# Performance work log

Measured on AMD Instinct MI355X. Metric: run time of the kernel, lower is better.

The kernel has to match this reference:

```python
import jax, jax.numpy as jnp
import numpy as np

PH = PW = 16  # patch size


def setup_inputs() -> dict:
    key = jax.random.key(0)
    k1, k2, k3, k4, k5 = jax.random.split(key, 5)
    B, N, D, V = 8, 4096, 768, 10240
    x = jax.random.uniform(k1, (B, N, D), dtype=jnp.float32)          # (B, N, ph*pw*C) in [0,1)
    patch_coord = jax.random.randint(k2, (B, N, 2), 0, 64).astype(jnp.int64)  # (y, x) grid coords
    patch_valid = jax.random.randint(k3, (B, N), 0, 2).astype(bool)
    proj_w = jax.random.normal(k4, (D, D), dtype=jnp.float32) * 0.02  # Linear weight (out, in), no bias
    pos_table = jax.random.normal(k5, (2, V, D), dtype=jnp.float32) * 0.02
    return {"x": x, "patch_coord": patch_coord, "patch_valid": patch_valid,
            "proj_w": proj_w, "pos_table": pos_table}


def reference(x, patch_coord, patch_valid, proj_w, pos_table):
    B, N, PPC = x.shape
    C = PPC // (PH * PW)
    # Reorder patch pixels from (ph, pw, C) flat order to (C, ph, pw) flat order.
    x = x.reshape(B, N, PH, PW, C).transpose(0, 1, 4, 2, 3).reshape(B, N, PPC)
    x = 2.0 * (x - 0.5)
    x = jnp.einsum('bnk,dk->bnd', x, proj_w)  # Linear, bias=False
    # External (y, x) -> internal (x, y)
    position_ids = patch_coord[..., ::-1]
    clamped = jnp.maximum(position_ids, 0)
    # Equivalent to one_hot(clamped) @ table summed over the 2 coord axes.
    pos = pos_table[0][clamped[..., 0]] + pos_table[1][clamped[..., 1]]  # (B, N, D)
    padding_positions = ~patch_valid
    pos = jnp.where(padding_positions[..., None], 0.0, pos)
    return x + pos, position_ids, padding_positions
```

## Files before the change

### kernel.cpp

```cpp
#include <hip/hip_runtime.h>
#include <hip/hip_bf16.h>
#include <cstddef>

#define D_DIM 768
#define V_DIM 10240
#define ROWS  32768
#define BM    64
#define BK    32
#define KTILES (D_DIM / BK)

using bf16x8 = __attribute__((ext_vector_type(8))) __bf16;
using bf16x4 = __attribute__((ext_vector_type(4))) __bf16;
using f32x4  = __attribute__((ext_vector_type(4))) float;

__global__ void prep_w(const float* __restrict__ W, __bf16* __restrict__ Wp,
                       float* __restrict__ bias) {
    __shared__ float row[D_DIM];
    __shared__ float red[256];
    const int d = blockIdx.x;
    const int t = threadIdx.x;
    float s = 0.f;
    for (int k = t; k < D_DIM; k += 256) {
        float w = W[(size_t)d * D_DIM + k];
        row[k] = w;
        s += w;
    }
    red[t] = s;
    __syncthreads();
    for (int off = 128; off > 0; off >>= 1) {
        if (t < off) red[t] += red[t + off];
        __syncthreads();
    }
    if (t == 0) bias[d] = -red[0];
    for (int j = t; j < D_DIM; j += 256) {
        int c  = j % 3;
        int pw = (j / 3) & 15;
        int ph = j / 48;
        Wp[(size_t)d * D_DIM + j] = (__bf16)(2.0f * row[c * 256 + ph * 16 + pw]);
    }
}

__launch_bounds__(512, 2)
__global__ void gemm_fused(const float* __restrict__ X, const __bf16* __restrict__ Wp,
                           const float* __restrict__ bias, const float* __restrict__ ptab,
                           const int* __restrict__ coord, const int* __restrict__ valid,
                           float* __restrict__ out0, float* __restrict__ out1,
                           float* __restrict__ out2) {
    __shared__ __align__(16) __bf16 la[2][BM * BK];
    __shared__ __align__(16) __bf16 lb[2][D_DIM * BK];

    const int tid  = threadIdx.x;
    const int lane = tid & 63;
    const int wave = tid >> 6;
    const int wr   = (wave >> 2) * 32;
    const int wc   = (wave & 3) * 192;
    const int lr   = lane & 15;
    const int qh   = lane >> 4;

    const int m0 = blockIdx.x * BM;

    if (tid < BM) {
        int m  = m0 + tid;
        int c0 = coord[2 * m];
        int c1 = coord[2 * m + 1];
        out1[2 * m]     = (float)c1;
        out1[2 * m + 1] = (float)c0;
        out2[m] = valid[m] ? 0.0f : 1.0f;
    }

    const __bf16* bsrc[6];
    int bdst[6];
    #pragma unroll
    for (int i = 0; i < 6; ++i) {
        int q   = i * 512 + tid;
        int row = q >> 2;
        int su  = (q & 3) ^ ((row >> 1) & 3);
        bsrc[i] = Wp + (size_t)row * D_DIM + su * 8;
        bdst[i] = q * 8;
    }

    const int a_row = tid >> 3;
    const int a_u   = (tid & 7) >> 1;
    const int a_h   = tid & 1;
    const int a_off = a_row * BK + (a_u ^ ((a_row >> 1) & 3)) * 8 + a_h * 4;
    const float* aptr = X + (size_t)(m0 + a_row) * D_DIM + ((tid & 7) << 2);

    int aoff[2], boff[12];
    #pragma unroll
    for (int i = 0; i < 2; ++i) {
        int row = wr + i * 16 + lr;
        aoff[i] = row * BK + (qh ^ ((row >> 1) & 3)) * 8;
    }
    #pragma unroll
    for (int j = 0; j < 12; ++j) {
        int row = wc + j * 16 + lr;
        boff[j] = row * BK + (qh ^ ((row >> 1) & 3)) * 8;
    }

    f32x4 acc[2][12] = {};

    #pragma unroll
    for (int i = 0; i < 6; ++i)
        __builtin_amdgcn_global_load_lds(
            (const __attribute__((address_space(1))) void*)bsrc[i],
            (__attribute__((address_space(3))) void*)&lb[0][bdst[i]], 16, 0, 0);
    {
        float4 f = *(const float4*)aptr;
        bf16x4 v;
        v[0] = (__bf16)f.x; v[1] = (__bf16)f.y; v[2] = (__bf16)f.z; v[3] = (__bf16)f.w;
        *(bf16x4*)&la[0][a_off] = v;
    }
    __syncthreads();

    for (int kt = 0; kt < KTILES; ++kt) {
        const int cur = kt & 1;
        const int nxt = cur ^ 1;
        const int k1  = (kt + 1) * BK;

        float4 fA;
        if (kt + 1 < KTILES) {
            #pragma unroll
            for (int i = 0; i < 6; ++i)
                __builtin_amdgcn_global_load_lds(
                    (const __attribute__((address_space(1))) void*)(bsrc[i] + k1),
                    (__attribute__((address_space(3))) void*)&lb[nxt][bdst[i]], 16, 0, 0);
            fA = *(const float4*)(aptr + k1);
        }

        bf16x8 af0 = *(const bf16x8*)&la[cur][aoff[0]];
        bf16x8 af1 = *(const bf16x8*)&la[cur][aoff[1]];

        #pragma unroll
        for (int j = 0; j < 12; ++j) {
            bf16x8 bfv = *(const bf16x8*)&lb[cur][boff[j]];
            acc[0][j] = __builtin_amdgcn_mfma_f32_16x16x32_bf16(af0, bfv, acc[0][j], 0, 0, 0);
            acc[1][j] = __builtin_amdgcn_mfma_f32_16x16x32_bf16(af1, bfv, acc[1][j], 0, 0, 0);
        }

        if (kt + 1 < KTILES) {
            bf16x4 v;
            v[0] = (__bf16)fA.x; v[1] = (__bf16)fA.y; v[2] = (__bf16)fA.z; v[3] = (__bf16)fA.w;
            *(bf16x4*)&la[nxt][a_off] = v;
        }
        __syncthreads();
    }

    const float* pt0 = ptab;
    const float* pt1 = ptab + (size_t)V_DIM * D_DIM;

    float bv[12];
    #pragma unroll
    for (int j = 0; j < 12; ++j)
        bv[j] = bias[wc + j * 16 + lr];

    #pragma unroll
    for (int i = 0; i < 2; ++i) {
        #pragma unroll
        for (int r = 0; r < 4; ++r) {
            const int m = m0 + wr + i * 16 + qh * 4 + r;
            int c0 = coord[2 * m];
            int c1 = coord[2 * m + 1];
            if (c0 < 0) c0 = 0;
            if (c1 < 0) c1 = 0;
            const int vld = valid[m];
            const float* p0 = pt0 + (size_t)c1 * D_DIM;
            const float* p1 = pt1 + (size_t)c0 * D_DIM;
            float* orow = out0 + (size_t)m * D_DIM;
            #pragma unroll
            for (int j = 0; j < 12; ++j) {
                const int d = wc + j * 16 + lr;
                float v = acc[i][j][r] + bv[j];
                if (vld)
                    v += p0[d] + p1[d];
                orow[d] = v;
            }
        }
    }
}

extern "C" void kernel_launch(void* const* d_in, const int* in_sizes, int n_in,
                              void* d_out, int out_size, void* d_ws, size_t ws_size,
                              hipStream_t stream) {
    const float* x     = (const float*)d_in[0];
    const int*   coord = (const int*)d_in[1];
    const int*   valid = (const int*)d_in[2];
    const float* W     = (const float*)d_in[3];
    const float* ptab  = (const float*)d_in[4];

    float* out0 = (float*)d_out;
    float* out1 = out0 + (size_t)ROWS * D_DIM;
    float* out2 = out1 + (size_t)ROWS * 2;

    __bf16* Wp   = (__bf16*)d_ws;
    float*  bias = (float*)((char*)d_ws + (size_t)D_DIM * D_DIM * sizeof(__bf16));

    hipLaunchKernelGGL(prep_w, dim3(D_DIM), dim3(256), 0, stream, W, Wp, bias);
    hipLaunchKernelGGL(gemm_fused, dim3(ROWS / BM), dim3(512), 0, stream,
                       x, Wp, bias, ptab, coord, valid, out0, out1, out2);
}
```

Before: 293.7 us.

## Split GEMM output columns across two blocks and raise occupancy

Each block now computes a 64x384 output tile instead of a full 64x768 row band, which halves the B-tile shared memory and the accumulator count. This lets launch bounds request 4 blocks per CU instead of 2. Block IDs are remapped so both column halves of a row band run close together, improving L2 reuse of X. The main loop is also unrolled by two with fixed buffers. The trade-off is that X rows are loaded and converted twice, once per column half.

```diff
diff --git a/kernel.cpp b/kernel.cpp
--- a/kernel.cpp
+++ b/kernel.cpp
@@ -6,6 +6,7 @@
 #define V_DIM 10240
 #define ROWS  32768
 #define BM    64
+#define BN    384
 #define BK    32
 #define KTILES (D_DIM / BK)
 
@@ -40,26 +41,31 @@
     }
 }
 
-__launch_bounds__(512, 2)
+__launch_bounds__(512, 4)
 __global__ void gemm_fused(const float* __restrict__ X, const __bf16* __restrict__ Wp,
                            const float* __restrict__ bias, const float* __restrict__ ptab,
                            const int* __restrict__ coord, const int* __restrict__ valid,
                            float* __restrict__ out0, float* __restrict__ out1,
                            float* __restrict__ out2) {
     __shared__ __align__(16) __bf16 la[2][BM * BK];
-    __shared__ __align__(16) __bf16 lb[2][D_DIM * BK];
+    __shared__ __align__(16) __bf16 lb[2][BN * BK];
 
     const int tid  = threadIdx.x;
     const int lane = tid & 63;
     const int wave = tid >> 6;
     const int wr   = (wave >> 2) * 32;
-    const int wc   = (wave & 3) * 192;
+    const int wc   = (wave & 3) * 96;
     const int lr   = lane & 15;
     const int qh   = lane >> 4;
 
-    const int m0 = blockIdx.x * BM;
-
-    if (tid < BM) {
+    const int id = blockIdx.x;
+    const int w  = (id & 7) * 128 + (id >> 3);
+    const int bx = w & 1;
+    const int by = w >> 1;
+    const int m0 = by * BM;
+    const int n0 = bx * BN;
+
+    if (bx == 0 && tid < BM) {
         int m  = m0 + tid;
         int c0 = coord[2 * m];
         int c1 = coord[2 * m + 1];
@@ -68,90 +74,92 @@
         out2[m] = valid[m] ? 0.0f : 1.0f;
     }
 
-    const __bf16* bsrc[6];
-    int bdst[6];
-    #pragma unroll
-    for (int i = 0; i < 6; ++i) {
-        int q   = i * 512 + tid;
-        int row = q >> 2;
-        int su  = (q & 3) ^ ((row >> 1) & 3);
-        bsrc[i] = Wp + (size_t)row * D_DIM + su * 8;
-        bdst[i] = q * 8;
+    const __bf16* bsrc0; const __bf16* bsrc1; const __bf16* bsrc2;
+    int bdst0, bdst1, bdst2;
+    {
+        int q, row, su;
+        q = tid;           row = q >> 2; su = (q & 3) ^ ((row >> 1) & 3);
+        bsrc0 = Wp + (size_t)(n0 + row) * D_DIM + su * 8;  bdst0 = q * 8;
+        q = 512 + tid;     row = q >> 2; su = (q & 3) ^ ((row >> 1) & 3);
+        bsrc1 = Wp + (size_t)(n0 + row) * D_DIM + su * 8;  bdst1 = q * 8;
+        q = 1024 + tid;    row = q >> 2; su = (q & 3) ^ ((row >> 1) & 3);
+        bsrc2 = Wp + (size_t)(n0 + row) * D_DIM + su * 8;  bdst2 = q * 8;
     }
 
     const int a_row = tid >> 3;
     const int a_u   = (tid & 7) >> 1;
     const int a_h   = tid & 1;
     const int a_off = a_row * BK + (a_u ^ ((a_row >> 1) & 3)) * 8 + a_h * 4;
-    const float* aptr = X + (size_t)(m0 + a_row) * D_DIM + ((tid & 7) << 2);
-
-    int aoff[2], boff[12];
+    const float* asrc = X + (size_t)(m0 + a_row) * D_DIM + ((tid & 7) << 2);
+
+    int aoff0, aoff1, boff[6];
+    {
+        int row = wr + lr;
+        aoff0 = row * BK + (qh ^ ((row >> 1) & 3)) * 8;
+        row = wr + 16 + lr;
+        aoff1 = row * BK + (qh ^ ((row >> 1) & 3)) * 8;
+    }
     #pragma unroll
-    for (int i = 0; i < 2; ++i) {
-        int row = wr + i * 16 + lr;
-        aoff[i] = row * BK + (qh ^ ((row >> 1) & 3)) * 8;
-    }
-    #pragma unroll
-    for (int j = 0; j < 12; ++j) {
+    for (int j = 0; j < 6; ++j) {
         int row = wc + j * 16 + lr;
         boff[j] = row * BK + (qh ^ ((row >> 1) & 3)) * 8;
     }
 
-    f32x4 acc[2][12] = {};
-
-    #pragma unroll
-    for (int i = 0; i < 6; ++i)
-        __builtin_amdgcn_global_load_lds(
-            (const __attribute__((address_space(1))) void*)bsrc[i],
-            (__attribute__((address_space(3))) void*)&lb[0][bdst[i]], 16, 0, 0);
-    {
-        float4 f = *(const float4*)aptr;
-        bf16x4 v;
-        v[0] = (__bf16)f.x; v[1] = (__bf16)f.y; v[2] = (__bf16)f.z; v[3] = (__bf16)f.w;
-        *(bf16x4*)&la[0][a_off] = v;
-    }
+    f32x4 acc[2][6] = {};
+
+#define STAGE(BUF, KT)                                                          \
+    do {                                                                        \
+        const int k0_ = (KT) * BK;                                              \
+        __builtin_amdgcn_global_load_lds(                                       \
+            (const __attribute__((address_space(1))) void*)(bsrc0 + k0_),       \
+            (__attribute__((address_space(3))) void*)&lb[BUF][bdst0], 16, 0, 0);\
+        __builtin_amdgcn_global_load_lds(                                       \
+            (const __attribute__((address_space(1))) void*)(bsrc1 + k0_),       \
+            (__attribute__((address_space(3))) void*)&lb[BUF][bdst1], 16, 0, 0);\
+        __builtin_amdgcn_global_load_lds(                                       \
+            (const __attribute__((address_space(1))) void*)(bsrc2 + k0_),       \
+            (__attribute__((address_space(3))) void*)&lb[BUF][bdst2], 16, 0, 0);\
+        float4 f_ = *(const float4*)(asrc + k0_);                               \
+        bf16x4 v_;                                                              \
+        v_[0] = (__bf16)f_.x; v_[1] = (__bf16)f_.y;                             \
+        v_[2] = (__bf16)f_.z; v_[3] = (__bf16)f_.w;                             \
+        *(bf16x4*)&la[BUF][a_off] = v_;                                         \
+    } while (0)
+
+#define COMPUTE(BUF)                                                            \
+    do {                                                                        \
+        bf16x8 af0_ = *(const bf16x8*)&la[BUF][aoff0];                          \
+        bf16x8 af1_ = *(const bf16x8*)&la[BUF][aoff1];                          \
+        _Pragma("unroll")                                                       \
+        for (int j = 0; j < 6; ++j) {                                           \
+            bf16x8 bv_ = *(const bf16x8*)&lb[BUF][boff[j]];                     \
+            acc[0][j] = __builtin_amdgcn_mfma_f32_16x16x32_bf16(af0_, bv_, acc[0][j], 0, 0, 0); \
+            acc[1][j] = __builtin_amdgcn_mfma_f32_16x16x32_bf16(af1_, bv_, acc[1][j], 0, 0, 0); \
+        }                                                                       \
+    } while (0)
+
+    STAGE(0, 0);
     __syncthreads();
 
-    for (int kt = 0; kt < KTILES; ++kt) {
-        const int cur = kt & 1;
-        const int nxt = cur ^ 1;
-        const int k1  = (kt + 1) * BK;
-
-        float4 fA;
-        if (kt + 1 < KTILES) {
-            #pragma unroll
-            for (int i = 0; i < 6; ++i)
-                __builtin_amdgcn_global_load_lds(
-                    (const __attribute__((address_space(1))) void*)(bsrc[i] + k1),
-                    (__attribute__((address_space(3))) void*)&lb[nxt][bdst[i]], 16, 0, 0);
-            fA = *(const float4*)(aptr + k1);
-        }
-
-        bf16x8 af0 = *(const bf16x8*)&la[cur][aoff[0]];
-        bf16x8 af1 = *(const bf16x8*)&la[cur][aoff[1]];
-
-        #pragma unroll
-        for (int j = 0; j < 12; ++j) {
-            bf16x8 bfv = *(const bf16x8*)&lb[cur][boff[j]];
-            acc[0][j] = __builtin_amdgcn_mfma_f32_16x16x32_bf16(af0, bfv, acc[0][j], 0, 0, 0);
-            acc[1][j] = __builtin_amdgcn_mfma_f32_16x16x32_bf16(af1, bfv, acc[1][j], 0, 0, 0);
-        }
-
-        if (kt + 1 < KTILES) {
-            bf16x4 v;
-            v[0] = (__bf16)fA.x; v[1] = (__bf16)fA.y; v[2] = (__bf16)fA.z; v[3] = (__bf16)fA.w;
-            *(bf16x4*)&la[nxt][a_off] = v;
-        }
+    for (int kt = 0; kt < KTILES; kt += 2) {
+        STAGE(1, kt + 1);
+        COMPUTE(0);
         __syncthreads();
-    }
+        if (kt + 2 < KTILES) STAGE(0, kt + 2);
+        COMPUTE(1);
+        __syncthreads();
+    }
+
+#undef STAGE
+#undef COMPUTE
 
     const float* pt0 = ptab;
     const float* pt1 = ptab + (size_t)V_DIM * D_DIM;
 
-    float bv[12];
+    float bv[6];
     #pragma unroll
-    for (int j = 0; j < 12; ++j)
-        bv[j] = bias[wc + j * 16 + lr];
+    for (int j = 0; j < 6; ++j)
+        bv[j] = bias[n0 + wc + j * 16 + lr];
 
     #pragma unroll
     for (int i = 0; i < 2; ++i) {
@@ -167,8 +175,8 @@
             const float* p1 = pt1 + (size_t)c0 * D_DIM;
             float* orow = out0 + (size_t)m * D_DIM;
             #pragma unroll
-            for (int j = 0; j < 12; ++j) {
-                const int d = wc + j * 16 + lr;
+            for (int j = 0; j < 6; ++j) {
+                const int d = n0 + wc + j * 16 + lr;
                 float v = acc[i][j][r] + bv[j];
                 if (vld)
                     v += p0[d] + p1[d];
@@ -195,6 +203,6 @@
     float*  bias = (float*)((char*)d_ws + (size_t)D_DIM * D_DIM * sizeof(__bf16));
 
     hipLaunchKernelGGL(prep_w, dim3(D_DIM), dim3(256), 0, stream, W, Wp, bias);
-    hipLaunchKernelGGL(gemm_fused, dim3(ROWS / BM), dim3(512), 0, stream,
+    hipLaunchKernelGGL(gemm_fused, dim3((ROWS / BM) * (D_DIM / BN)), dim3(512), 0, stream,
                        x, Wp, bias, ptab, coord, valid, out0, out1, out2);
 }
```

Result: slower. 309.2 us (+5.3%).

## Keep weight column stripe resident in LDS and stream A directly from global

Applied to the files above, without the earlier changes.

Replaces the K-tiled double-buffered GEMM, which staged both A and the full weight through LDS, with a persistent-style grid of 256 blocks. Each block loads a 96-column stripe of the bf16 weight into LDS once and then processes 1024 rows in four panels. A fragments are read straight from global fp32 memory and converted in registers, which removes per-tile LDS staging and barriers. The block index mapping groups 8 stripes over the same rows so the X reads can hit in L2. The cost is that each X row is now read by 8 different blocks, every A load goes directly to global memory without prefetch, and only 256 blocks run, which may leave the device underused.

```diff
diff --git a/kernel.cpp b/kernel.cpp
--- a/kernel.cpp
+++ b/kernel.cpp
@@ -5,12 +5,12 @@
 #define D_DIM 768
 #define V_DIM 10240
 #define ROWS  32768
-#define BM    64
-#define BK    32
-#define KTILES (D_DIM / BK)
+#define BN    96
+#define PR    256
+#define PANELS 4
+#define KTILES 24
 
 using bf16x8 = __attribute__((ext_vector_type(8))) __bf16;
-using bf16x4 = __attribute__((ext_vector_type(4))) __bf16;
 using f32x4  = __attribute__((ext_vector_type(4))) float;
 
 __global__ void prep_w(const float* __restrict__ W, __bf16* __restrict__ Wp,
@@ -41,138 +41,125 @@
 }
 
 __launch_bounds__(512, 2)
-__global__ void gemm_fused(const float* __restrict__ X, const __bf16* __restrict__ Wp,
-                           const float* __restrict__ bias, const float* __restrict__ ptab,
-                           const int* __restrict__ coord, const int* __restrict__ valid,
-                           float* __restrict__ out0, float* __restrict__ out1,
-                           float* __restrict__ out2) {
-    __shared__ __align__(16) __bf16 la[2][BM * BK];
-    __shared__ __align__(16) __bf16 lb[2][D_DIM * BK];
+__global__ void gemm_resident(const float* __restrict__ X, const __bf16* __restrict__ Wp,
+                              const float* __restrict__ bias, const float* __restrict__ ptab,
+                              const int* __restrict__ coord, const int* __restrict__ valid,
+                              float* __restrict__ out0, float* __restrict__ out1,
+                              float* __restrict__ out2) {
+    __shared__ __align__(16) __bf16 lb[BN * D_DIM];
 
     const int tid  = threadIdx.x;
     const int lane = tid & 63;
     const int wave = tid >> 6;
-    const int wr   = (wave >> 2) * 32;
-    const int wc   = (wave & 3) * 192;
     const int lr   = lane & 15;
     const int qh   = lane >> 4;
 
-    const int m0 = blockIdx.x * BM;
+    const int b      = blockIdx.x;
+    const int x      = b & 7;
+    const int i      = b >> 3;
+    const int stripe = i & 7;
+    const int rowblk = x * 4 + (i >> 3);
+    const int n0     = stripe * BN;
+    const size_t mbase = (size_t)rowblk * (PR * PANELS);
 
-    if (tid < BM) {
-        int m  = m0 + tid;
-        int c0 = coord[2 * m];
-        int c1 = coord[2 * m + 1];
-        out1[2 * m]     = (float)c1;
-        out1[2 * m + 1] = (float)c0;
-        out2[m] = valid[m] ? 0.0f : 1.0f;
+    #pragma unroll
+    for (int u = 0; u < 18; ++u) {
+        int q   = u * 512 + tid;
+        int row = q / 96;
+        int un  = q - row * 96;
+        int su  = un ^ (row & 7);
+        const __bf16* src = Wp + (size_t)(n0 + row) * D_DIM + su * 8;
+        __builtin_amdgcn_global_load_lds(
+            (const __attribute__((address_space(1))) void*)src,
+            (__attribute__((address_space(3))) void*)&lb[q * 8], 16, 0, 0);
     }
 
-    const __bf16* bsrc[6];
-    int bdst[6];
-    #pragma unroll
-    for (int i = 0; i < 6; ++i) {
-        int q   = i * 512 + tid;
-        int row = q >> 2;
-        int su  = (q & 3) ^ ((row >> 1) & 3);
-        bsrc[i] = Wp + (size_t)row * D_DIM + su * 8;
-        bdst[i] = q * 8;
+    if (stripe == 0) {
+        #pragma unroll
+        for (int t = 0; t < 2; ++t) {
+            size_t m = mbase + t * 512 + tid;
+            int c0 = coord[2 * m];
+            int c1 = coord[2 * m + 1];
+            out1[2 * m]     = (float)c1;
+            out1[2 * m + 1] = (float)c0;
+            out2[m] = valid[m] ? 0.0f : 1.0f;
+        }
     }
 
-    const int a_row = tid >> 3;
-    const int a_u   = (tid & 7) >> 1;
-    const int a_h   = tid & 1;
-    const int a_off = a_row * BK + (a_u ^ ((a_row >> 1) & 3)) * 8 + a_h * 4;
-    const float* aptr = X + (size_t)(m0 + a_row) * D_DIM + ((tid & 7) << 2);
+    float bv[6];
+    #pragma unroll
+    for (int j = 0; j < 6; ++j)
+        bv[j] = bias[n0 + j * 16 + lr];
 
-    int aoff[2], boff[12];
+    int brow[6], bx7[6];
     #pragma unroll
-    for (int i = 0; i < 2; ++i) {
-        int row = wr + i * 16 + lr;
-        aoff[i] = row * BK + (qh ^ ((row >> 1) & 3)) * 8;
-    }
-    #pragma unroll
-    for (int j = 0; j < 12; ++j) {
-        int row = wc + j * 16 + lr;
-        boff[j] = row * BK + (qh ^ ((row >> 1) & 3)) * 8;
+    for (int j = 0; j < 6; ++j) {
+        int row = j * 16 + lr;
+        brow[j] = row * D_DIM;
+        bx7[j]  = row & 7;
     }
 
-    f32x4 acc[2][12] = {};
-
-    #pragma unroll
-    for (int i = 0; i < 6; ++i)
-        __builtin_amdgcn_global_load_lds(
-            (const __attribute__((address_space(1))) void*)bsrc[i],
-            (__attribute__((address_space(3))) void*)&lb[0][bdst[i]], 16, 0, 0);
-    {
-        float4 f = *(const float4*)aptr;
-        bf16x4 v;
-        v[0] = (__bf16)f.x; v[1] = (__bf16)f.y; v[2] = (__bf16)f.z; v[3] = (__bf16)f.w;
-        *(bf16x4*)&la[0][a_off] = v;
-    }
     __syncthreads();
-
-    for (int kt = 0; kt < KTILES; ++kt) {
-        const int cur = kt & 1;
-        const int nxt = cur ^ 1;
-        const int k1  = (kt + 1) * BK;
-
-        float4 fA;
-        if (kt + 1 < KTILES) {
-            #pragma unroll
-            for (int i = 0; i < 6; ++i)
-                __builtin_amdgcn_global_load_lds(
-                    (const __attribute__((address_space(1))) void*)(bsrc[i] + k1),
-                    (__attribute__((address_space(3))) void*)&lb[nxt][bdst[i]], 16, 0, 0);
-            fA = *(const float4*)(aptr + k1);
-        }
-
-        bf16x8 af0 = *(const bf16x8*)&la[cur][aoff[0]];
-        bf16x8 af1 = *(const bf16x8*)&la[cur][aoff[1]];
-
-        #pragma unroll
-        for (int j = 0; j < 12; ++j) {
-            bf16x8 bfv = *(const bf16x8*)&lb[cur][boff[j]];
-            acc[0][j] = __builtin_amdgcn_mfma_f32_16x16x32_bf16(af0, bfv, acc[0][j], 0, 0, 0);
-            acc[1][j] = __builtin_amdgcn_mfma_f32_16x16x32_bf16(af1, bfv, acc[1][j], 0, 0, 0);
-        }
-
-        if (kt + 1 < KTILES) {
-            bf16x4 v;
-            v[0] = (__bf16)fA.x; v[1] = (__bf16)fA.y; v[2] = (__bf16)fA.z; v[3] = (__bf16)fA.w;
-            *(bf16x4*)&la[nxt][a_off] = v;
-        }
-        __syncthreads();
-    }
 
     const float* pt0 = ptab;
     const float* pt1 = ptab + (size_t)V_DIM * D_DIM;
 
-    float bv[12];
-    #pragma unroll
-    for (int j = 0; j < 12; ++j)
-        bv[j] = bias[wc + j * 16 + lr];
+    for (int p = 0; p < PANELS; ++p) {
+        const size_t m0 = mbase + (size_t)p * PR;
+        const size_t wrow = m0 + wave * 32;
 
-    #pragma unroll
-    for (int i = 0; i < 2; ++i) {
+        const float* a0 = X + (wrow + lr) * D_DIM + qh * 8;
+        const float* a1 = a0 + (size_t)16 * D_DIM;
+
+        f32x4 acc[2][6] = {};
+
+        #pragma unroll 8
+        for (int kt = 0; kt < KTILES; ++kt) {
+            const float4 f00 = *(const float4*)(a0 + kt * 32);
+            const float4 f01 = *(const float4*)(a0 + kt * 32 + 4);
+            const float4 f10 = *(const float4*)(a1 + kt * 32);
+            const float4 f11 = *(const float4*)(a1 + kt * 32 + 4);
+            bf16x8 af0, af1;
+            af0[0] = (__bf16)f00.x; af0[1] = (__bf16)f00.y;
+            af0[2] = (__bf16)f00.z; af0[3] = (__bf16)f00.w;
+            af0[4] = (__bf16)f01.x; af0[5] = (__bf16)f01.y;
+            af0[6] = (__bf16)f01.z; af0[7] = (__bf16)f01.w;
+            af1[0] = (__bf16)f10.x; af1[1] = (__bf16)f10.y;
+            af1[2] = (__bf16)f10.z; af1[3] = (__bf16)f10.w;
+            af1[4] = (__bf16)f11.x; af1[5] = (__bf16)f11.y;
+            af1[6] = (__bf16)f11.z; af1[7] = (__bf16)f11.w;
+
+            const int ku = (kt << 2) | qh;
+            #pragma unroll
+            for (int j = 0; j < 6; ++j) {
+                const int un = ku ^ bx7[j];
+                const bf16x8 bfv = *(const bf16x8*)&lb[brow[j] + un * 8];
+                acc[0][j] = __builtin_amdgcn_mfma_f32_16x16x32_bf16(af0, bfv, acc[0][j], 0, 0, 0);
+                acc[1][j] = __builtin_amdgcn_mfma_f32_16x16x32_bf16(af1, bfv, acc[1][j], 0, 0, 0);
+            }
+        }
+
         #pragma unroll
-        for (int r = 0; r < 4; ++r) {
-            const int m = m0 + wr + i * 16 + qh * 4 + r;
-            int c0 = coord[2 * m];
-            int c1 = coord[2 * m + 1];
-            if (c0 < 0) c0 = 0;
-            if (c1 < 0) c1 = 0;
-            const int vld = valid[m];
-            const float* p0 = pt0 + (size_t)c1 * D_DIM;
-            const float* p1 = pt1 + (size_t)c0 * D_DIM;
-            float* orow = out0 + (size_t)m * D_DIM;
+        for (int ii = 0; ii < 2; ++ii) {
             #pragma unroll
-            for (int j = 0; j < 12; ++j) {
-                const int d = wc + j * 16 + lr;
-                float v = acc[i][j][r] + bv[j];
-                if (vld)
-                    v += p0[d] + p1[d];
-                orow[d] = v;
+            for (int r = 0; r < 4; ++r) {
+                const size_t m = wrow + ii * 16 + qh * 4 + r;
+                int c0 = coord[2 * m];
+                int c1 = coord[2 * m + 1];
+                if (c0 < 0) c0 = 0;
+                if (c1 < 0) c1 = 0;
+                const int vld = valid[m];
+                const float* p0 = pt0 + (size_t)c1 * D_DIM + n0;
+                const float* p1 = pt1 + (size_t)c0 * D_DIM + n0;
+                float* orow = out0 + m * D_DIM + n0;
+                #pragma unroll
+                for (int j = 0; j < 6; ++j) {
+                    const int d = j * 16 + lr;
+                    float v = acc[ii][j][r] + bv[j];
+                    if (vld)
+                        v += p0[d] + p1[d];
+                    orow[d] = v;
+                }
             }
         }
     }
@@ -195,6 +182,6 @@
     float*  bias = (float*)((char*)d_ws + (size_t)D_DIM * D_DIM * sizeof(__bf16));
 
     hipLaunchKernelGGL(prep_w, dim3(D_DIM), dim3(256), 0, stream, W, Wp, bias);
-    hipLaunchKernelGGL(gemm_fused, dim3(ROWS / BM), dim3(512), 0, stream,
+    hipLaunchKernelGGL(gemm_resident, dim3(256), dim3(512), 0, stream,
                        x, Wp, bias, ptab, coord, valid, out0, out1, out2);
 }
```

Result: slower. 323.3 us (+10.1%).

## Retile GEMM to 128x128 blocks with XCD-aware block mapping, single-buffered

Applied to the files above, without the earlier changes.

Replaces the 64-row by full-768-column tile with 128x128 output tiles over a 2D grid, using 256 threads, each wave computing a 64x64 sub-tile. Block IDs are remapped so blocks on the same XCD share the same rows of X, which is meant to improve L2 reuse of X. The double-buffered prefetch is dropped in favour of a single buffer with two barriers per k-step. X is now reloaded and converted to bf16 once per column tile (6 times instead of once), and the lost overlap may expose load latency.

```diff
diff --git a/kernel.cpp b/kernel.cpp
--- a/kernel.cpp
+++ b/kernel.cpp
@@ -4,13 +4,12 @@
 
 #define D_DIM 768
 #define V_DIM 10240
-#define ROWS  32768
-#define BM    64
-#define BK    32
-#define KTILES (D_DIM / BK)
+#define ROWS 32768
+#define BM 128
+#define BN 128
+#define BK 32
 
 using bf16x8 = __attribute__((ext_vector_type(8))) __bf16;
-using bf16x4 = __attribute__((ext_vector_type(4))) __bf16;
 using f32x4  = __attribute__((ext_vector_type(4))) float;
 
 __global__ void prep_w(const float* __restrict__ W, __bf16* __restrict__ Wp,
@@ -40,26 +39,32 @@
     }
 }
 
-__launch_bounds__(512, 2)
+__launch_bounds__(256)
 __global__ void gemm_fused(const float* __restrict__ X, const __bf16* __restrict__ Wp,
                            const float* __restrict__ bias, const float* __restrict__ ptab,
                            const int* __restrict__ coord, const int* __restrict__ valid,
                            float* __restrict__ out0, float* __restrict__ out1,
                            float* __restrict__ out2) {
-    __shared__ __align__(16) __bf16 la[2][BM * BK];
-    __shared__ __align__(16) __bf16 lb[2][D_DIM * BK];
+    __shared__ __align__(16) __bf16 la[BM * BK];
+    __shared__ __align__(16) __bf16 lb[BN * BK];
+
+    const int id  = blockIdx.x;
+    const int xcd = id & 7;
+    const int j6  = id >> 3;
+    const int p   = xcd * 32 + j6 / 6;
+    const int c   = j6 % 6;
+    const int m0  = p * BM;
+    const int n0  = c * BN;
 
     const int tid  = threadIdx.x;
     const int lane = tid & 63;
     const int wave = tid >> 6;
-    const int wr   = (wave >> 2) * 32;
-    const int wc   = (wave & 3) * 192;
+    const int wr   = (wave >> 1) * 64;
+    const int wc   = (wave & 1) * 64;
     const int lr   = lane & 15;
     const int qh   = lane >> 4;
 
-    const int m0 = blockIdx.x * BM;
-
-    if (tid < BM) {
+    if (c == 0 && tid < BM) {
         int m  = m0 + tid;
         int c0 = coord[2 * m];
         int c1 = coord[2 * m + 1];
@@ -68,111 +73,102 @@
         out2[m] = valid[m] ? 0.0f : 1.0f;
     }
 
-    const __bf16* bsrc[6];
-    int bdst[6];
+    const float*  srcA[2];
+    const __bf16* srcB[2];
+    int dst[2];
     #pragma unroll
-    for (int i = 0; i < 6; ++i) {
-        int q   = i * 512 + tid;
+    for (int i = 0; i < 2; ++i) {
+        int q   = i * 256 + tid;
         int row = q >> 2;
-        int su  = (q & 3) ^ ((row >> 1) & 3);
-        bsrc[i] = Wp + (size_t)row * D_DIM + su * 8;
-        bdst[i] = q * 8;
+        int un  = (q & 3) ^ ((row >> 1) & 3);
+        srcA[i] = X  + (size_t)(m0 + row) * D_DIM + un * 8;
+        srcB[i] = Wp + (size_t)(n0 + row) * D_DIM + un * 8;
+        dst[i]  = q * 8;
     }
 
-    const int a_row = tid >> 3;
-    const int a_u   = (tid & 7) >> 1;
-    const int a_h   = tid & 1;
-    const int a_off = a_row * BK + (a_u ^ ((a_row >> 1) & 3)) * 8 + a_h * 4;
-    const float* aptr = X + (size_t)(m0 + a_row) * D_DIM + ((tid & 7) << 2);
-
-    int aoff[2], boff[12];
+    int aoff[4], boff[4];
     #pragma unroll
-    for (int i = 0; i < 2; ++i) {
-        int row = wr + i * 16 + lr;
-        aoff[i] = row * BK + (qh ^ ((row >> 1) & 3)) * 8;
-    }
-    #pragma unroll
-    for (int j = 0; j < 12; ++j) {
-        int row = wc + j * 16 + lr;
-        boff[j] = row * BK + (qh ^ ((row >> 1) & 3)) * 8;
+    for (int i = 0; i < 4; ++i) {
+        int rowa = wr + i * 16 + lr;
+        aoff[i] = rowa * BK + ((qh ^ ((rowa >> 1) & 3)) * 8);
+        int rowb = wc + i * 16 + lr;
+        boff[i] = rowb * BK + ((qh ^ ((rowb >> 1) & 3)) * 8);
     }
 
-    f32x4 acc[2][12] = {};
+    f32x4 acc[4][4] = {};
 
-    #pragma unroll
-    for (int i = 0; i < 6; ++i)
-        __builtin_amdgcn_global_load_lds(
-            (const __attribute__((address_space(1))) void*)bsrc[i],
-            (__attribute__((address_space(3))) void*)&lb[0][bdst[i]], 16, 0, 0);
-    {
-        float4 f = *(const float4*)aptr;
-        bf16x4 v;
-        v[0] = (__bf16)f.x; v[1] = (__bf16)f.y; v[2] = (__bf16)f.z; v[3] = (__bf16)f.w;
-        *(bf16x4*)&la[0][a_off] = v;
-    }
-    __syncthreads();
+    for (int kt = 0; kt < D_DIM / BK; ++kt) {
+        const int k0 = kt * BK;
 
-    for (int kt = 0; kt < KTILES; ++kt) {
-        const int cur = kt & 1;
-        const int nxt = cur ^ 1;
-        const int k1  = (kt + 1) * BK;
+        #pragma unroll
+        for (int i = 0; i < 2; ++i)
+            __builtin_amdgcn_global_load_lds(
+                (const __attribute__((address_space(1))) void*)(srcB[i] + k0),
+                (__attribute__((address_space(3))) void*)&lb[dst[i]], 16, 0, 0);
 
-        float4 fA;
-        if (kt + 1 < KTILES) {
-            #pragma unroll
-            for (int i = 0; i < 6; ++i)
-                __builtin_amdgcn_global_load_lds(
-                    (const __attribute__((address_space(1))) void*)(bsrc[i] + k1),
-                    (__attribute__((address_space(3))) void*)&lb[nxt][bdst[i]], 16, 0, 0);
-            fA = *(const float4*)(aptr + k1);
+        {
+            float4 f00 = *(const float4*)(srcA[0] + k0);
+            float4 f01 = *(const float4*)(srcA[0] + k0 + 4);
+            float4 f10 = *(const float4*)(srcA[1] + k0);
+            float4 f11 = *(const float4*)(srcA[1] + k0 + 4);
+            bf16x8 v0, v1;
+            v0[0] = (__bf16)f00.x; v0[1] = (__bf16)f00.y;
+            v0[2] = (__bf16)f00.z; v0[3] = (__bf16)f00.w;
+            v0[4] = (__bf16)f01.x; v0[5] = (__bf16)f01.y;
+            v0[6] = (__bf16)f01.z; v0[7] = (__bf16)f01.w;
+            v1[0] = (__bf16)f10.x; v1[1] = (__bf16)f10.y;
+            v1[2] = (__bf16)f10.z; v1[3] = (__bf16)f10.w;
+            v1[4] = (__bf16)f11.x; v1[5] = (__bf16)f11.y;
+            v1[6] = (__bf16)f11.z; v1[7] = (__bf16)f11.w;
+            *(bf16x8*)&la[dst[0]] = v0;
+            *(bf16x8*)&la[dst[1]] = v1;
         }
 
-        bf16x8 af0 = *(const bf16x8*)&la[cur][aoff[0]];
-        bf16x8 af1 = *(const bf16x8*)&la[cur][aoff[1]];
+        __syncthreads();
+
+        bf16x8 af[4], bfr[4];
+        #pragma unroll
+        for (int i = 0; i < 4; ++i)
+            af[i] = *(const bf16x8*)&la[aoff[i]];
+        #pragma unroll
+        for (int j = 0; j < 4; ++j)
+            bfr[j] = *(const bf16x8*)&lb[boff[j]];
 
         #pragma unroll
-        for (int j = 0; j < 12; ++j) {
-            bf16x8 bfv = *(const bf16x8*)&lb[cur][boff[j]];
-            acc[0][j] = __builtin_amdgcn_mfma_f32_16x16x32_bf16(af0, bfv, acc[0][j], 0, 0, 0);
-            acc[1][j] = __builtin_amdgcn_mfma_f32_16x16x32_bf16(af1, bfv, acc[1][j], 0, 0, 0);
-        }
+        for (int i = 0; i < 4; ++i)
+            #pragma unroll
+            for (int j = 0; j < 4; ++j)
+                acc[i][j] = __builtin_amdgcn_mfma_f32_16x16x32_bf16(af[i], bfr[j], acc[i][j], 0, 0, 0);
 
-        if (kt + 1 < KTILES) {
-            bf16x4 v;
-            v[0] = (__bf16)fA.x; v[1] = (__bf16)fA.y; v[2] = (__bf16)fA.z; v[3] = (__bf16)fA.w;
-            *(bf16x4*)&la[nxt][a_off] = v;
-        }
         __syncthreads();
     }
 
     const float* pt0 = ptab;
     const float* pt1 = ptab + (size_t)V_DIM * D_DIM;
+    const int rq = (lane >> 4) * 4;
 
-    float bv[12];
+    float bvals[4];
     #pragma unroll
-    for (int j = 0; j < 12; ++j)
-        bv[j] = bias[wc + j * 16 + lr];
+    for (int j = 0; j < 4; ++j)
+        bvals[j] = bias[n0 + wc + j * 16 + lr];
 
     #pragma unroll
-    for (int i = 0; i < 2; ++i) {
+    for (int i = 0; i < 4; ++i) {
         #pragma unroll
         for (int r = 0; r < 4; ++r) {
-            const int m = m0 + wr + i * 16 + qh * 4 + r;
+            int m = m0 + wr + i * 16 + rq + r;
             int c0 = coord[2 * m];
             int c1 = coord[2 * m + 1];
             if (c0 < 0) c0 = 0;
             if (c1 < 0) c1 = 0;
-            const int vld = valid[m];
-            const float* p0 = pt0 + (size_t)c1 * D_DIM;
-            const float* p1 = pt1 + (size_t)c0 * D_DIM;
-            float* orow = out0 + (size_t)m * D_DIM;
+            int vld = valid[m];
             #pragma unroll
-            for (int j = 0; j < 12; ++j) {
-                const int d = wc + j * 16 + lr;
-                float v = acc[i][j][r] + bv[j];
+            for (int j = 0; j < 4; ++j) {
+                int d = n0 + wc + j * 16 + lr;
+                float v = acc[i][j][r] + bvals[j];
                 if (vld)
-                    v += p0[d] + p1[d];
-                orow[d] = v;
+                    v += pt0[(size_t)c1 * D_DIM + d] + pt1[(size_t)c0 * D_DIM + d];
+                out0[(size_t)m * D_DIM + d] = v;
             }
         }
     }
@@ -195,6 +191,6 @@
     float*  bias = (float*)((char*)d_ws + (size_t)D_DIM * D_DIM * sizeof(__bf16));
 
     hipLaunchKernelGGL(prep_w, dim3(D_DIM), dim3(256), 0, stream, W, Wp, bias);
-    hipLaunchKernelGGL(gemm_fused, dim3(ROWS / BM), dim3(512), 0, stream,
+    hipLaunchKernelGGL(gemm_fused, dim3((ROWS / BM) * (D_DIM / BN)), dim3(256), 0, stream,
                        x, Wp, bias, ptab, coord, valid, out0, out1, out2);
 }
```

After: 288.3 us. Within noise of the previous version (-1.8%).
